# Kernel tuning notes

Measured on AMD Instinct MI355X. Metric: run time of the kernel, lower is better.

Reference implementation:

```python
import jax, jax.numpy as jnp
import numpy as np
import math

B, S, D, H, MAX_LEN = 4, 1024, 1024, 16, 1024
DH = D // H  # 64

def setup_inputs() -> dict:
    key = jax.random.key(0)
    ks = jax.random.split(key, 9)
    s = 1.0 / math.sqrt(D)
    return {
        "q":  jax.random.normal(ks[0], (B, S, D), jnp.float32),
        "kv": jax.random.normal(ks[1], (B, S, D), jnp.float32),
        "Wq": jax.random.normal(ks[2], (D, D), jnp.float32) * s,
        "bq": jax.random.normal(ks[3], (D,), jnp.float32) * s,
        "Wk": jax.random.normal(ks[4], (D, D), jnp.float32) * s,
        "bk": jax.random.normal(ks[5], (D,), jnp.float32) * s,
        "Wv": jax.random.normal(ks[6], (D, D), jnp.float32) * s,
        "bv": jax.random.normal(ks[7], (D,), jnp.float32) * s,
        "Er": jax.random.normal(ks[8], (MAX_LEN, DH), jnp.float32),
    }

def _skew(QEr):
    # QEr: [B, H, S, S]. Music-Transformer skew trick:
    # pad one zero column on the left, reshape, drop first row.
    b, h, r, c = QEr.shape
    padded = jnp.pad(QEr, ((0, 0), (0, 0), (0, 0), (1, 0)))  # [b,h,r,c+1]
    reshaped = padded.reshape(b, h, c + 1, r)
    return reshaped[:, :, 1:, :]  # [b,h,r,c]

def reference(q, kv, Wq, bq, Wk, bk, Wv, bv, Er):
    b, s, d = kv.shape
    # projections (nn.Linear: x @ W + b with W stored [in,out])
    k = (kv @ Wk + bk).reshape(b, s, H, DH).transpose(0, 2, 3, 1)  # [b,h,dh,s]
    v = (kv @ Wv + bv).reshape(b, s, H, DH).transpose(0, 2, 1, 3)  # [b,h,s,dh]
    qh = (q @ Wq + bq).reshape(b, s, H, DH).transpose(0, 2, 1, 3)  # [b,h,s,dh]
    # relative position scores
    Er_t = Er[MAX_LEN - s:, :].T            # [dh, s]
    QEr = jnp.einsum('bhsd,dt->bhst', qh, Er_t)
    Srel = _skew(QEr)                        # [b,h,s,s]
    # content scores
    QK = jnp.einsum('bhsd,bhdt->bhst', qh, k)
    attn = (QK + Srel) / math.sqrt(DH)
    causal = jnp.tril(jnp.ones((s, s), dtype=bool))[None, None]
    attn = jnp.where(causal, attn, -jnp.inf)
    attn = jax.nn.softmax(attn, axis=-1)
    out = jnp.einsum('bhst,bhtd->bhsd', attn, v)
    out = out.transpose(0, 2, 1, 3).reshape(b, s, d)
    return out  # dropout is identity (p=0 / eval)
```

## Files before the change

kernel.cpp:

```cpp
#include <hip/hip_runtime.h>
#include <hip/hip_bf16.h>

typedef __bf16 bf16x8 __attribute__((ext_vector_type(8)));
typedef __bf16 bf16x4 __attribute__((ext_vector_type(4)));
typedef float  f32x4  __attribute__((ext_vector_type(4)));
typedef unsigned __attribute__((may_alias)) u32a;

#define MFMA_B16(a, b, c) __builtin_amdgcn_mfma_f32_16x16x32_bf16((a), (b), (c), 0, 0, 0)

static constexpr int Bk  = 4;
static constexpr int Sk  = 1024;
static constexpr int Dk  = 1024;
static constexpr int Hk  = 16;
static constexpr int DHk = 64;

static constexpr size_t QH_OFF = 0;
static constexpr size_t K_OFF  = 4194304;
static constexpr size_t VT_OFF = 8388608;
static constexpr size_t WT_OFF = 12582912;
static constexpr size_t ER_OFF = 15728640;
static constexpr size_t WS_ELEMS = 15794176;

__device__ __forceinline__ void load_lds16(const void* g, void* l) {
    __builtin_amdgcn_global_load_lds((const __attribute__((address_space(1))) void*)g,
                                     (__attribute__((address_space(3))) void*)l, 16, 0, 0);
}

template<int CTRL>
__device__ __forceinline__ float dppf(float x) {
    int v = __builtin_bit_cast(int, x);
    return __builtin_bit_cast(float,
        __builtin_amdgcn_update_dpp(v, v, CTRL, 0xF, 0xF, false));
}
__device__ __forceinline__ float rmax16(float x) {
    x = fmaxf(x, dppf<0x128>(x));
    x = fmaxf(x, dppf<0x124>(x));
    x = fmaxf(x, dppf<0x122>(x));
    x = fmaxf(x, dppf<0x121>(x));
    return x;
}
__device__ __forceinline__ float rsum16(float x) {
    x += dppf<0x128>(x);
    x += dppf<0x124>(x);
    x += dppf<0x122>(x);
    x += dppf<0x121>(x);
    return x;
}
__device__ __forceinline__ unsigned pk_bf16(float lo, float hi) {
    unsigned r;
    asm("v_cvt_pk_bf16_f32 %0, %1, %2" : "=v"(r) : "v"(lo), "v"(hi));
    return r;
}

__global__ void prep_kernel(const float* __restrict__ Wq, const float* __restrict__ Wk,
                            const float* __restrict__ Wv, const float* __restrict__ Er,
                            __bf16* __restrict__ wt, __bf16* __restrict__ erb)
{
    __shared__ float tile[64][65];
    const int z = blockIdx.z;
    const int tid = threadIdx.x;
    if (z == 3) {
        int idx = (blockIdx.y * 16 + blockIdx.x) * 256 + tid;
        erb[idx] = (__bf16)Er[idx];
        return;
    }
    const float* W = (z == 0) ? Wq : (z == 1 ? Wk : Wv);
    __bf16* dst = wt + (size_t)z * Dk * Dk;
    const int k0 = blockIdx.y * 64, n0 = blockIdx.x * 64;
    #pragma unroll
    for (int j = 0; j < 16; ++j) {
        int idx = tid + j * 256; int r = idx >> 6, c = idx & 63;
        tile[r][c] = W[(size_t)(k0 + r) * Dk + n0 + c];
    }
    __syncthreads();
    #pragma unroll
    for (int j = 0; j < 16; ++j) {
        int idx = tid + j * 256; int r = idx >> 6, c = idx & 63;
        dst[(size_t)(n0 + r) * Dk + k0 + c] = (__bf16)tile[c][r];
    }
}

__global__ __launch_bounds__(256) void proj_kernel(
    const float* __restrict__ Xq, const float* __restrict__ Xkv,
    const float* __restrict__ bq, const float* __restrict__ bk,
    const float* __restrict__ bv, const __bf16* __restrict__ wt,
    __bf16* __restrict__ qh, __bf16* __restrict__ kws, __bf16* __restrict__ vt)
{
    __shared__ __align__(16) float  Al[128 * 32];
    __shared__ __align__(16) __bf16 Bl[128 * 32];

    const int z = blockIdx.z;
    const float* X    = (z == 0) ? Xq : Xkv;
    const float* bias = (z == 0) ? bq : (z == 1 ? bk : bv);
    const __bf16* Wz  = wt + (size_t)z * Dk * Dk;

    const int m0   = blockIdx.x * 128;
    const int n0   = blockIdx.y * 128;
    const int tid  = threadIdx.x;
    const int lane = tid & 63;
    const int w    = tid >> 6;
    const int wr   = w >> 1, wc = w & 1;
    const int l15  = lane & 15;
    const int g    = lane >> 4;

    const float* asrc[4];
    int adst[4];
    #pragma unroll
    for (int i = 0; i < 4; ++i) {
        const int c = w * 4 + i;
        asrc[i] = X + (size_t)(m0 + c * 8 + (lane >> 3)) * Dk + (((lane & 7) ^ (lane >> 3)) << 2);
        adst[i] = c * 1024 + lane * 16;
    }
    const __bf16* bsrc[2];
    int bdst[2];
    #pragma unroll
    for (int i = 0; i < 2; ++i) {
        const int c = w * 2 + i;
        bsrc[i] = Wz + (size_t)(n0 + c * 16 + (lane >> 2)) * Dk + (((lane & 3) ^ ((lane >> 3) & 3)) << 3);
        bdst[i] = c * 1024 + lane * 16;
    }

    int aoff0[4], aoff1[4], boff[4];
    #pragma unroll
    for (int m = 0; m < 4; ++m) {
        const int row = wr * 64 + m * 16 + l15;
        aoff0[m] = row * 128 + (((2 * g)     ^ (l15 & 7)) << 4);
        aoff1[m] = row * 128 + (((2 * g + 1) ^ (l15 & 7)) << 4);
    }
    #pragma unroll
    for (int n = 0; n < 4; ++n) {
        const int row = wc * 64 + n * 16 + l15;
        boff[n] = row * 64 + ((g ^ ((l15 >> 1) & 3)) << 4);
    }

    const f32x4 fz = {0.f, 0.f, 0.f, 0.f};
    f32x4 acc[4][4];
    #pragma unroll
    for (int m = 0; m < 4; ++m)
        #pragma unroll
        for (int n = 0; n < 4; ++n) acc[m][n] = fz;

    const char* Alc = (const char*)Al;
    const char* Blc = (const char*)Bl;

    for (int ks = 0; ks < Dk / 32; ++ks) {
        #pragma unroll
        for (int i = 0; i < 4; ++i)
            load_lds16(asrc[i], (char*)Al + adst[i]);
        #pragma unroll
        for (int i = 0; i < 2; ++i)
            load_lds16(bsrc[i], (char*)Bl + bdst[i]);
        #pragma unroll
        for (int i = 0; i < 4; ++i) asrc[i] += 32;
        #pragma unroll
        for (int i = 0; i < 2; ++i) bsrc[i] += 32;
        __syncthreads();

        bf16x8 bf[4];
        #pragma unroll
        for (int n = 0; n < 4; ++n)
            bf[n] = *(const bf16x8*)(Blc + boff[n]);
        bf16x8 af[4];
        #pragma unroll
        for (int m = 0; m < 4; ++m) {
            f32x4 x0 = *(const f32x4*)(Alc + aoff0[m]);
            f32x4 x1 = *(const f32x4*)(Alc + aoff1[m]);
            bf16x8 a;
            a[0] = (__bf16)x0[0]; a[1] = (__bf16)x0[1]; a[2] = (__bf16)x0[2]; a[3] = (__bf16)x0[3];
            a[4] = (__bf16)x1[0]; a[5] = (__bf16)x1[1]; a[6] = (__bf16)x1[2]; a[7] = (__bf16)x1[3];
            af[m] = a;
        }

        #pragma unroll
        for (int m = 0; m < 4; ++m)
            #pragma unroll
            for (int n = 0; n < 4; ++n)
                acc[m][n] = MFMA_B16(af[m], bf[n], acc[m][n]);
        __syncthreads();
    }

    #pragma unroll
    for (int n = 0; n < 4; ++n) {
        const float bb = bias[n0 + wc * 64 + n * 16 + l15];
        #pragma unroll
        for (int m = 0; m < 4; ++m)
            #pragma unroll
            for (int r = 0; r < 4; ++r) acc[m][n][r] += bb;
    }

    const int b   = m0 >> 10;
    const int s0t = (m0 & 1023) + wr * 64;
    const int h   = (n0 + wc * 64) >> 6;

    if (z < 2) {
        __bf16* dst = (z == 0) ? qh : kws;
        const size_t rowbase = (size_t)(b * Hk + h) * Sk;
        #pragma unroll
        for (int m = 0; m < 4; ++m) {
            #pragma unroll
            for (int r = 0; r < 4; ++r) {
                const int s = s0t + m * 16 + g * 4 + r;
                __bf16* drow = dst + (rowbase + s) * DHk;
                #pragma unroll
                for (int n = 0; n < 4; ++n)
                    drow[n * 16 + l15] = (__bf16)acc[m][n][r];
            }
        }
    } else {
        const size_t hb = (size_t)(b * Hk + h) * DHk;
        #pragma unroll
        for (int m = 0; m < 4; ++m) {
            const int sb = s0t + m * 16 + g * 4;
            #pragma unroll
            for (int n = 0; n < 4; ++n) {
                const int dh = n * 16 + l15;
                bf16x4 pk;
                #pragma unroll
                for (int r = 0; r < 4; ++r) pk[r] = (__bf16)acc[m][n][r];
                *(bf16x4*)(vt + (hb + dh) * Sk + sb) = pk;
            }
        }
    }
}

__global__ __launch_bounds__(256, 3) void attn_kernel(
    const __bf16* __restrict__ qh, const __bf16* __restrict__ kws,
    const __bf16* __restrict__ vt, const __bf16* __restrict__ erb,
    float* __restrict__ out)
{
    __shared__ __align__(16) __bf16 Kl[2][4096];
    __shared__ __align__(16) __bf16 Vl[2][4096];
    __shared__ __align__(16) __bf16 P_lds[4][16][88];

    const int tid  = threadIdx.x;
    const int lane = tid & 63;
    const int w    = tid >> 6;
    const int l15  = lane & 15;
    const int g    = lane >> 4;

    const int lid   = blockIdx.x;
    const int bh    = lid & 63;
    const int strip = 15 - (lid >> 6);
    const int ntw   = strip + 1;
    const int sw    = strip * 64 + w * 16;

    const __bf16* kbase = kws + (size_t)bh * Sk * DHk;
    const __bf16* vbase = vt  + (size_t)bh * DHk * Sk;
    const __bf16* qbase = qh  + ((size_t)bh * Sk + sw) * DHk;

    __bf16 (*Pw)[88] = P_lds[w];

    const int trow   = tid >> 3;
    const int tslot  = tid & 7;
    const int srcoff = (tslot ^ (trow & 7)) << 3;
    char* kd0 = (char*)Kl + tid * 16;
    char* vd0 = (char*)Vl + tid * 16;

    bf16x8 aq[2];
    aq[0] = *(const bf16x8*)(qbase + l15 * DHk + g * 8);
    aq[1] = *(const bf16x8*)(qbase + l15 * DHk + 32 + g * 8);

    const f32x4 fz = {0.f, 0.f, 0.f, 0.f};
    f32x4 O[4];
    float m_[4], l_[4];
    #pragma unroll
    for (int n = 0; n < 4; ++n) O[n] = fz;
    #pragma unroll
    for (int r = 0; r < 4; ++r) { m_[r] = -1e30f; l_[r] = 0.f; }

    const float SCL = 0.125f * 1.44269504088896f;

    load_lds16(kbase + (size_t)trow * DHk + srcoff,        kd0);
    load_lds16(kbase + (size_t)(32 + trow) * DHk + srcoff, kd0 + 4096);
    load_lds16(vbase + (size_t)trow * Sk + srcoff,         vd0);
    load_lds16(vbase + (size_t)(32 + trow) * Sk + srcoff,  vd0 + 4096);

    for (int it = 0; it < ntw; ++it) {
        const int t0  = it * 64;
        const int cur = it & 1;

        __builtin_amdgcn_sched_barrier(0);
        __builtin_amdgcn_s_barrier();
        __builtin_amdgcn_sched_barrier(0);
        if (it + 1 < ntw) {
            const int t0n = t0 + 64;
            char* kd = kd0 + (cur ^ 1) * 8192;
            char* vd = vd0 + (cur ^ 1) * 8192;
            load_lds16(kbase + (size_t)(t0n + trow) * DHk + srcoff,      kd);
            load_lds16(kbase + (size_t)(t0n + 32 + trow) * DHk + srcoff, kd + 4096);
            load_lds16(vbase + (size_t)trow * Sk + t0n + srcoff,         vd);
            load_lds16(vbase + (size_t)(32 + trow) * Sk + t0n + srcoff,  vd + 4096);
            asm volatile("s_waitcnt vmcnt(4)" ::: "memory");
        } else {
            asm volatile("s_waitcnt vmcnt(0)" ::: "memory");
        }
        __builtin_amdgcn_sched_barrier(0);
        __builtin_amdgcn_s_barrier();
        __builtin_amdgcn_sched_barrier(0);

        const char* Kc = (const char*)Kl + cur * 8192;
        const char* Vc = (const char*)Vl + cur * 8192;

        const int jb = t0 - sw + 1008;
        bf16x8 ec[10];
        #pragma unroll
        for (int kt = 0; kt < 2; ++kt)
            #pragma unroll
            for (int jj = 0; jj < 5; ++jj) {
                int jr = jb + jj * 16 + l15;
                jr = (jr > 1023) ? 1023 : jr;
                ec[kt * 5 + jj] = *(const bf16x8*)(erb + (size_t)jr * DHk + kt * 32 + g * 8);
            }

        f32x4 sc[4];
        #pragma unroll
        for (int j = 0; j < 4; ++j) sc[j] = fz;
        #pragma unroll
        for (int kt = 0; kt < 2; ++kt) {
            bf16x8 kb[4];
            #pragma unroll
            for (int j = 0; j < 4; ++j)
                kb[j] = *(const bf16x8*)(Kc + (j * 16 + l15) * 128 + ((((kt << 2) | g) ^ (l15 & 7)) << 4));
            __builtin_amdgcn_s_setprio(1);
            #pragma unroll
            for (int j = 0; j < 4; ++j)
                sc[j] = MFMA_B16(aq[kt], kb[j], sc[j]);
            __builtin_amdgcn_s_setprio(0);
        }

        f32x4 gf[5];
        #pragma unroll
        for (int jj = 0; jj < 5; ++jj) gf[jj] = fz;
        __builtin_amdgcn_s_setprio(1);
        #pragma unroll
        for (int kt = 0; kt < 2; ++kt)
            #pragma unroll
            for (int jj = 0; jj < 5; ++jj)
                gf[jj] = MFMA_B16(aq[kt], ec[kt * 5 + jj], gf[jj]);
        __builtin_amdgcn_s_setprio(0);

        #pragma unroll
        for (int r = 0; r < 4; ++r) {
            const int rr  = g * 4 + r;
            const int sft = 15 - rr;
            const int src = (g << 4) + ((l15 + sft) & 15);
            const bool hi = (l15 + sft) >= 16;
            float h[5];
            #pragma unroll
            for (int jj = 0; jj < 5; ++jj) h[jj] = __shfl(gf[jj][r], src);
            const int s = sw + rr;
            #pragma unroll
            for (int j = 0; j < 4; ++j) {
                float gval = hi ? h[j + 1] : h[j];
                float v = (sc[j][r] + gval) * SCL;
                int t = t0 + j * 16 + l15;
                sc[j][r] = (t > s) ? -1e30f : v;
            }
        }

        float mt[4];
        #pragma unroll
        for (int r = 0; r < 4; ++r)
            mt[r] = rmax16(fmaxf(fmaxf(sc[0][r], sc[1][r]), fmaxf(sc[2][r], sc[3][r])));

        bool grow = (mt[0] > m_[0] + 8.f) || (mt[1] > m_[1] + 8.f) ||
                    (mt[2] > m_[2] + 8.f) || (mt[3] > m_[3] + 8.f);
        if (__any(grow)) {
            #pragma unroll
            for (int r = 0; r < 4; ++r) {
                float mnew = fmaxf(m_[r], mt[r]);
                float scl  = exp2f(m_[r] - mnew);
                l_[r] *= scl;
                m_[r]  = mnew;
                #pragma unroll
                for (int n = 0; n < 4; ++n) O[n][r] *= scl;
            }
        }
        #pragma unroll
        for (int r = 0; r < 4; ++r) {
            float rs = 0.f;
            #pragma unroll
            for (int j = 0; j < 4; ++j) {
                float p = exp2f(sc[j][r] - m_[r]);
                sc[j][r] = p; rs += p;
            }
            l_[r] += rsum16(rs);
        }

        {
            const int p01 = l15 & 1;
            #pragma unroll
            for (int j = 0; j < 4; ++j) {
                #pragma unroll
                for (int h2 = 0; h2 < 2; ++h2) {
                    float a0 = sc[j][h2];
                    float a2 = sc[j][h2 + 2];
                    float b0 = dppf<0xB1>(a0);
                    float b2 = dppf<0xB1>(a2);
                    float lo = p01 ? b2 : a0;
                    float hi = p01 ? a2 : b0;
                    unsigned wd = pk_bf16(lo, hi);
                    const int row = g * 4 + h2 + (p01 ? 2 : 0);
                    *(u32a*)(&Pw[row][(j << 4) + (l15 & ~1)]) = wd;
                }
            }
        }
        asm volatile("" ::: "memory");
        __builtin_amdgcn_sched_barrier(0);

        __builtin_amdgcn_s_setprio(1);
        #pragma unroll
        for (int kt = 0; kt < 2; ++kt) {
            bf16x8 pa = *(const bf16x8*)(&Pw[l15][kt * 32 + g * 8]);
            #pragma unroll
            for (int n = 0; n < 4; ++n) {
                bf16x8 vbf = *(const bf16x8*)(Vc + (n * 16 + l15) * 128 + ((((kt << 2) | g) ^ (l15 & 7)) << 4));
                O[n] = MFMA_B16(pa, vbf, O[n]);
            }
        }
        __builtin_amdgcn_s_setprio(0);
    }

    const int b = bh >> 4, h = bh & 15;
    float* obase = out + ((size_t)b * Sk + sw) * Dk + h * DHk;
    #pragma unroll
    for (int r = 0; r < 4; ++r) {
        float inv = 1.f / l_[r];
        #pragma unroll
        for (int n = 0; n < 4; ++n)
            obase[(size_t)(g * 4 + r) * Dk + n * 16 + l15] = O[n][r] * inv;
    }
}

extern "C" void kernel_launch(void* const* d_in, const int* in_sizes, int n_in,
                              void* d_out, int out_size, void* d_ws, size_t ws_size,
                              hipStream_t stream)
{
    const float* q  = (const float*)d_in[0];
    const float* kv = (const float*)d_in[1];
    const float* Wq = (const float*)d_in[2];
    const float* bq = (const float*)d_in[3];
    const float* Wk = (const float*)d_in[4];
    const float* bk = (const float*)d_in[5];
    const float* Wv = (const float*)d_in[6];
    const float* bv = (const float*)d_in[7];
    const float* Er = (const float*)d_in[8];
    float* out = (float*)d_out;

    if (ws_size < WS_ELEMS * sizeof(__bf16)) return;
    __bf16* ws  = (__bf16*)d_ws;
    __bf16* qh  = ws + QH_OFF;
    __bf16* kws = ws + K_OFF;
    __bf16* vt  = ws + VT_OFF;
    __bf16* wt  = ws + WT_OFF;
    __bf16* erb = ws + ER_OFF;

    prep_kernel<<<dim3(16, 16, 4), 256, 0, stream>>>(Wq, Wk, Wv, Er, wt, erb);
    proj_kernel<<<dim3(32, 8, 3), 256, 0, stream>>>(q, kv, bq, bk, bv, wt, qh, kws, vt);
    attn_kernel<<<dim3(1024), 256, 0, stream>>>(qh, kws, vt, erb, out);
}
```

Measured before the change: 103.4 us.

## Process 32 query rows per wave to reuse K/V tiles across two sub-tiles

Each wave now handles two 16-row query sub-tiles, so each block covers 128 query rows. K and V fragments loaded from LDS feed twice as many MFMAs, and the grid is halved to 512 blocks. Waves whose rows lie entirely before the current key tile skip compute via an early continue but still take part in the barriers. The cost is more registers per thread (two O, m and l sets), fewer blocks for load balancing across the causal triangle, and some wasted iterations for waves in the lower half of each strip.

```diff
diff --git a/kernel.cpp b/kernel.cpp
--- a/kernel.cpp
+++ b/kernel.cpp
@@ -230,7 +230,7 @@
 {
     __shared__ __align__(16) __bf16 Kl[2][4096];
     __shared__ __align__(16) __bf16 Vl[2][4096];
-    __shared__ __align__(16) __bf16 P_lds[4][16][88];
+    __shared__ __align__(16) __bf16 P_lds[4][32][72];
 
     const int tid  = threadIdx.x;
     const int lane = tid & 63;
@@ -240,15 +240,15 @@
 
     const int lid   = blockIdx.x;
     const int bh    = lid & 63;
-    const int strip = 15 - (lid >> 6);
-    const int ntw   = strip + 1;
-    const int sw    = strip * 64 + w * 16;
+    const int strip = 7 - (lid >> 6);
+    const int ntw   = 2 * strip + 2;
+    const int sw    = strip * 128 + w * 32;
 
     const __bf16* kbase = kws + (size_t)bh * Sk * DHk;
     const __bf16* vbase = vt  + (size_t)bh * DHk * Sk;
     const __bf16* qbase = qh  + ((size_t)bh * Sk + sw) * DHk;
 
-    __bf16 (*Pw)[88] = P_lds[w];
+    __bf16 (*Pw)[72] = P_lds[w];
 
     const int trow   = tid >> 3;
     const int tslot  = tid & 7;
@@ -256,17 +256,23 @@
     char* kd0 = (char*)Kl + tid * 16;
     char* vd0 = (char*)Vl + tid * 16;
 
-    bf16x8 aq[2];
-    aq[0] = *(const bf16x8*)(qbase + l15 * DHk + g * 8);
-    aq[1] = *(const bf16x8*)(qbase + l15 * DHk + 32 + g * 8);
+    bf16x8 aq[2][2];
+    #pragma unroll
+    for (int h = 0; h < 2; ++h) {
+        aq[h][0] = *(const bf16x8*)(qbase + (16 * h + l15) * DHk + g * 8);
+        aq[h][1] = *(const bf16x8*)(qbase + (16 * h + l15) * DHk + 32 + g * 8);
+    }
 
     const f32x4 fz = {0.f, 0.f, 0.f, 0.f};
-    f32x4 O[4];
-    float m_[4], l_[4];
-    #pragma unroll
-    for (int n = 0; n < 4; ++n) O[n] = fz;
-    #pragma unroll
-    for (int r = 0; r < 4; ++r) { m_[r] = -1e30f; l_[r] = 0.f; }
+    f32x4 O[2][4];
+    float m_[2][4], l_[2][4];
+    #pragma unroll
+    for (int h = 0; h < 2; ++h) {
+        #pragma unroll
+        for (int n = 0; n < 4; ++n) O[h][n] = fz;
+        #pragma unroll
+        for (int r = 0; r < 4; ++r) { m_[h][r] = -1e30f; l_[h][r] = 0.f; }
+    }
 
     const float SCL = 0.125f * 1.44269504088896f;
 
@@ -298,23 +304,16 @@
         __builtin_amdgcn_s_barrier();
         __builtin_amdgcn_sched_barrier(0);
 
+        if (t0 > sw + 31) continue;
+
         const char* Kc = (const char*)Kl + cur * 8192;
         const char* Vc = (const char*)Vl + cur * 8192;
 
-        const int jb = t0 - sw + 1008;
-        bf16x8 ec[10];
-        #pragma unroll
-        for (int kt = 0; kt < 2; ++kt)
-            #pragma unroll
-            for (int jj = 0; jj < 5; ++jj) {
-                int jr = jb + jj * 16 + l15;
-                jr = (jr > 1023) ? 1023 : jr;
-                ec[kt * 5 + jj] = *(const bf16x8*)(erb + (size_t)jr * DHk + kt * 32 + g * 8);
-            }
-
-        f32x4 sc[4];
-        #pragma unroll
-        for (int j = 0; j < 4; ++j) sc[j] = fz;
+        f32x4 sc[2][4];
+        #pragma unroll
+        for (int h = 0; h < 2; ++h)
+            #pragma unroll
+            for (int j = 0; j < 4; ++j) sc[h][j] = fz;
         #pragma unroll
         for (int kt = 0; kt < 2; ++kt) {
             bf16x8 kb[4];
@@ -323,85 +322,101 @@
                 kb[j] = *(const bf16x8*)(Kc + (j * 16 + l15) * 128 + ((((kt << 2) | g) ^ (l15 & 7)) << 4));
             __builtin_amdgcn_s_setprio(1);
             #pragma unroll
-            for (int j = 0; j < 4; ++j)
-                sc[j] = MFMA_B16(aq[kt], kb[j], sc[j]);
+            for (int h = 0; h < 2; ++h)
+                #pragma unroll
+                for (int j = 0; j < 4; ++j)
+                    sc[h][j] = MFMA_B16(aq[h][kt], kb[j], sc[h][j]);
             __builtin_amdgcn_s_setprio(0);
         }
 
-        f32x4 gf[5];
-        #pragma unroll
-        for (int jj = 0; jj < 5; ++jj) gf[jj] = fz;
-        __builtin_amdgcn_s_setprio(1);
-        #pragma unroll
-        for (int kt = 0; kt < 2; ++kt)
-            #pragma unroll
-            for (int jj = 0; jj < 5; ++jj)
-                gf[jj] = MFMA_B16(aq[kt], ec[kt * 5 + jj], gf[jj]);
-        __builtin_amdgcn_s_setprio(0);
-
-        #pragma unroll
-        for (int r = 0; r < 4; ++r) {
-            const int rr  = g * 4 + r;
-            const int sft = 15 - rr;
-            const int src = (g << 4) + ((l15 + sft) & 15);
-            const bool hi = (l15 + sft) >= 16;
-            float h[5];
-            #pragma unroll
-            for (int jj = 0; jj < 5; ++jj) h[jj] = __shfl(gf[jj][r], src);
-            const int s = sw + rr;
-            #pragma unroll
-            for (int j = 0; j < 4; ++j) {
-                float gval = hi ? h[j + 1] : h[j];
-                float v = (sc[j][r] + gval) * SCL;
-                int t = t0 + j * 16 + l15;
-                sc[j][r] = (t > s) ? -1e30f : v;
-            }
-        }
-
-        float mt[4];
-        #pragma unroll
-        for (int r = 0; r < 4; ++r)
-            mt[r] = rmax16(fmaxf(fmaxf(sc[0][r], sc[1][r]), fmaxf(sc[2][r], sc[3][r])));
-
-        bool grow = (mt[0] > m_[0] + 8.f) || (mt[1] > m_[1] + 8.f) ||
-                    (mt[2] > m_[2] + 8.f) || (mt[3] > m_[3] + 8.f);
-        if (__any(grow)) {
+        #pragma unroll
+        for (int h = 0; h < 2; ++h) {
+            const int swh = sw + 16 * h;
+            const int jb  = t0 - swh + 1008;
+
+            f32x4 gf[5];
+            #pragma unroll
+            for (int jj = 0; jj < 5; ++jj) gf[jj] = fz;
+            #pragma unroll
+            for (int kt = 0; kt < 2; ++kt) {
+                bf16x8 ec[5];
+                #pragma unroll
+                for (int jj = 0; jj < 5; ++jj) {
+                    int jr = jb + jj * 16 + l15;
+                    jr = (jr > 1023) ? 1023 : jr;
+                    ec[jj] = *(const bf16x8*)(erb + (size_t)jr * DHk + kt * 32 + g * 8);
+                }
+                __builtin_amdgcn_s_setprio(1);
+                #pragma unroll
+                for (int jj = 0; jj < 5; ++jj)
+                    gf[jj] = MFMA_B16(aq[h][kt], ec[jj], gf[jj]);
+                __builtin_amdgcn_s_setprio(0);
+            }
+
             #pragma unroll
             for (int r = 0; r < 4; ++r) {
-                float mnew = fmaxf(m_[r], mt[r]);
-                float scl  = exp2f(m_[r] - mnew);
-                l_[r] *= scl;
-                m_[r]  = mnew;
-                #pragma unroll
-                for (int n = 0; n < 4; ++n) O[n][r] *= scl;
-            }
-        }
-        #pragma unroll
-        for (int r = 0; r < 4; ++r) {
-            float rs = 0.f;
-            #pragma unroll
-            for (int j = 0; j < 4; ++j) {
-                float p = exp2f(sc[j][r] - m_[r]);
-                sc[j][r] = p; rs += p;
-            }
-            l_[r] += rsum16(rs);
-        }
-
-        {
-            const int p01 = l15 & 1;
-            #pragma unroll
-            for (int j = 0; j < 4; ++j) {
-                #pragma unroll
-                for (int h2 = 0; h2 < 2; ++h2) {
-                    float a0 = sc[j][h2];
-                    float a2 = sc[j][h2 + 2];
-                    float b0 = dppf<0xB1>(a0);
-                    float b2 = dppf<0xB1>(a2);
-                    float lo = p01 ? b2 : a0;
-                    float hi = p01 ? a2 : b0;
-                    unsigned wd = pk_bf16(lo, hi);
-                    const int row = g * 4 + h2 + (p01 ? 2 : 0);
-                    *(u32a*)(&Pw[row][(j << 4) + (l15 & ~1)]) = wd;
+                const int rr  = g * 4 + r;
+                const int sft = 15 - rr;
+                const int src = (g << 4) + ((l15 + sft) & 15);
+                const bool hi = (l15 + sft) >= 16;
+                float hv[5];
+                #pragma unroll
+                for (int jj = 0; jj < 5; ++jj) hv[jj] = __shfl(gf[jj][r], src);
+                const int s = swh + rr;
+                #pragma unroll
+                for (int j = 0; j < 4; ++j) {
+                    float gval = hi ? hv[j + 1] : hv[j];
+                    float v = (sc[h][j][r] + gval) * SCL;
+                    int t = t0 + j * 16 + l15;
+                    sc[h][j][r] = (t > s) ? -1e30f : v;
+                }
+            }
+
+            float mt[4];
+            #pragma unroll
+            for (int r = 0; r < 4; ++r)
+                mt[r] = rmax16(fmaxf(fmaxf(sc[h][0][r], sc[h][1][r]),
+                                     fmaxf(sc[h][2][r], sc[h][3][r])));
+            bool grow = (mt[0] > m_[h][0] + 8.f) || (mt[1] > m_[h][1] + 8.f) ||
+                        (mt[2] > m_[h][2] + 8.f) || (mt[3] > m_[h][3] + 8.f);
+            if (__any(grow)) {
+                #pragma unroll
+                for (int r = 0; r < 4; ++r) {
+                    float mnew = fmaxf(m_[h][r], mt[r]);
+                    float scl  = exp2f(m_[h][r] - mnew);
+                    l_[h][r] *= scl;
+                    m_[h][r]  = mnew;
+                    #pragma unroll
+                    for (int n = 0; n < 4; ++n) O[h][n][r] *= scl;
+                }
+            }
+            #pragma unroll
+            for (int r = 0; r < 4; ++r) {
+                float rs = 0.f;
+                #pragma unroll
+                for (int j = 0; j < 4; ++j) {
+                    float p = exp2f(sc[h][j][r] - m_[h][r]);
+                    sc[h][j][r] = p; rs += p;
+                }
+                l_[h][r] += rsum16(rs);
+            }
+
+            {
+                const int p01 = l15 & 1;
+                #pragma unroll
+                for (int j = 0; j < 4; ++j) {
+                    #pragma unroll
+                    for (int h2 = 0; h2 < 2; ++h2) {
+                        float a0 = sc[h][j][h2];
+                        float a2 = sc[h][j][h2 + 2];
+                        float b0 = dppf<0xB1>(a0);
+                        float b2 = dppf<0xB1>(a2);
+                        float lo = p01 ? b2 : a0;
+                        float hi = p01 ? a2 : b0;
+                        unsigned wd = pk_bf16(lo, hi);
+                        const int row = 16 * h + g * 4 + h2 + (p01 ? 2 : 0);
+                        *(u32a*)(&Pw[row][(j << 4) + (l15 & ~1)]) = wd;
+                    }
                 }
             }
         }
@@ -411,24 +426,29 @@
         __builtin_amdgcn_s_setprio(1);
         #pragma unroll
         for (int kt = 0; kt < 2; ++kt) {
-            bf16x8 pa = *(const bf16x8*)(&Pw[l15][kt * 32 + g * 8]);
+            bf16x8 pa0 = *(const bf16x8*)(&Pw[l15][kt * 32 + g * 8]);
+            bf16x8 pa1 = *(const bf16x8*)(&Pw[16 + l15][kt * 32 + g * 8]);
             #pragma unroll
             for (int n = 0; n < 4; ++n) {
                 bf16x8 vbf = *(const bf16x8*)(Vc + (n * 16 + l15) * 128 + ((((kt << 2) | g) ^ (l15 & 7)) << 4));
-                O[n] = MFMA_B16(pa, vbf, O[n]);
+                O[0][n] = MFMA_B16(pa0, vbf, O[0][n]);
+                O[1][n] = MFMA_B16(pa1, vbf, O[1][n]);
             }
         }
         __builtin_amdgcn_s_setprio(0);
     }
 
-    const int b = bh >> 4, h = bh & 15;
-    float* obase = out + ((size_t)b * Sk + sw) * Dk + h * DHk;
-    #pragma unroll
-    for (int r = 0; r < 4; ++r) {
-        float inv = 1.f / l_[r];
-        #pragma unroll
-        for (int n = 0; n < 4; ++n)
-            obase[(size_t)(g * 4 + r) * Dk + n * 16 + l15] = O[n][r] * inv;
+    const int b = bh >> 4, hh = bh & 15;
+    float* obase = out + ((size_t)b * Sk + sw) * Dk + hh * DHk;
+    #pragma unroll
+    for (int h = 0; h < 2; ++h) {
+        #pragma unroll
+        for (int r = 0; r < 4; ++r) {
+            float inv = 1.f / l_[h][r];
+            #pragma unroll
+            for (int n = 0; n < 4; ++n)
+                obase[(size_t)(16 * h + g * 4 + r) * Dk + n * 16 + l15] = O[h][n][r] * inv;
+        }
     }
 }
 
@@ -457,5 +477,5 @@
 
     prep_kernel<<<dim3(16, 16, 4), 256, 0, stream>>>(Wq, Wk, Wv, Er, wt, erb);
     proj_kernel<<<dim3(32, 8, 3), 256, 0, stream>>>(q, kv, bq, bk, bv, wt, qh, kws, vt);
-    attn_kernel<<<dim3(1024), 256, 0, stream>>>(qh, kws, vt, erb, out);
-}
+    attn_kernel<<<dim3(512), 256, 0, stream>>>(qh, kws, vt, erb, out);
+}
```

Measured after the change: 155.9 us. 1.51x slower.
